# Kernel tuning notes

Hardware: AMD Instinct MI355X
Metric: run time of the kernel (lower is better)

## Reference

```python
import jax, jax.numpy as jnp
import numpy as np

N = 100000      # nodes
E = 1600000     # edges
F_IN = 256      # num_features
H = 128         # hidden_dim
C = 16          # num_classes
LOG_SIGMA0 = float(np.log(0.1))  # prior_sigma = 0.1


def setup_inputs() -> dict:
    key = jax.random.key(0)
    ks = jax.random.split(key, 8)
    x = jax.random.normal(ks[0], (N, F_IN), jnp.float32)
    edge_index = jax.random.randint(ks[1], (2, E), 0, N, dtype=jnp.int64)
    # GCNConv linear weight + bias
    W = jax.random.normal(ks[2], (F_IN, H), jnp.float32) / np.float32(np.sqrt(F_IN))
    gcn_b = jnp.zeros((H,), jnp.float32)
    # BayesLinear params (mu + log_sigma) and fixed sampled noise eps
    w_mu = jax.random.normal(ks[3], (C, H), jnp.float32) / np.float32(np.sqrt(H))
    w_log_sigma = jnp.full((C, H), LOG_SIGMA0, jnp.float32)
    b_mu = jnp.zeros((C,), jnp.float32)
    b_log_sigma = jnp.full((C,), LOG_SIGMA0, jnp.float32)
    eps_w = jax.random.normal(ks[4], (C, H), jnp.float32)
    eps_b = jax.random.normal(ks[5], (C,), jnp.float32)
    return {"x": x, "edge_index": edge_index, "W": W, "gcn_b": gcn_b,
            "w_mu": w_mu, "w_log_sigma": w_log_sigma,
            "b_mu": b_mu, "b_log_sigma": b_log_sigma,
            "eps_w": eps_w, "eps_b": eps_b}


def reference(x, edge_index, W, gcn_b, w_mu, w_log_sigma, b_mu, b_log_sigma, eps_w, eps_b):
    n = x.shape[0]
    # --- GCNConv: add self-loops, symmetric deg^{-1/2} normalization ---
    loop = jnp.arange(n, dtype=edge_index.dtype)
    src = jnp.concatenate([edge_index[0], loop])  # message source j
    dst = jnp.concatenate([edge_index[1], loop])  # aggregation target i
    deg = jax.ops.segment_sum(jnp.ones_like(dst, dtype=x.dtype), dst, num_segments=n)
    deg_inv_sqrt = jnp.where(deg > 0, jax.lax.rsqrt(deg), 0.0)
    norm = deg_inv_sqrt[src] * deg_inv_sqrt[dst]            # [E+N]
    h = x @ W                                               # [N,H] transform first
    msg = h[src] * norm[:, None]                            # [E+N,H] gather
    agg = jax.ops.segment_sum(msg, dst, num_segments=n)     # [N,H] scatter-add
    agg = agg + gcn_b
    # --- ReLU; dropout is identity in eval mode ---
    a = jax.nn.relu(agg)
    # --- BayesLinear: w = mu + exp(log_sigma) * eps ---
    w = w_mu + jnp.exp(w_log_sigma) * eps_w                 # [C,H]
    b = b_mu + jnp.exp(b_log_sigma) * eps_b                 # [C]
    logits = a @ w.T + b                                    # [N,C]
    return jax.nn.log_softmax(logits, axis=1)
```

## Files before the change

### kernel.cpp

```cpp
#include <hip/hip_runtime.h>
#include <hip/hip_bf16.h>

#define N_NODES 100000
#define F_IN    256
#define H_DIM   128
#define C_CLS   16
#define NB_SCAN ((N_NODES + 255) / 256)
#define NSHARD  8
#define SHARD_W ((N_NODES + NSHARD - 1) / NSHARD)

typedef __attribute__((ext_vector_type(8))) short  short8;
typedef __attribute__((ext_vector_type(4))) float  float4v;
typedef __attribute__((ext_vector_type(4))) unsigned short ushort4v;

__device__ __forceinline__ float b2f(ushort u) {
    union { unsigned int i; float f; } v;
    v.i = ((unsigned int)u) << 16;
    return v.f;
}

__device__ __forceinline__ ushort f2b(float f) {
    unsigned int x = __float_as_uint(f);
    unsigned int r = (x + 0x7FFFu + ((x >> 16) & 1u)) >> 16;
    return (ushort)r;
}

__device__ __forceinline__ float ldsel(const void* p, int i, int f32f) {
    return f32f ? ((const float*)p)[i] : b2f(((const ushort*)p)[i]);
}

__global__ __launch_bounds__(64) void sniff(const ushort* __restrict__ x,
                                            const int* __restrict__ ei,
                                            int* __restrict__ flags) {
    int lane = threadIdx.x;
    int cnt_bf = 0;
#pragma unroll
    for (int j = 0; j < 4; ++j) {
        ushort u = x[lane * 4 + j];
        int e = (u >> 7) & 0xFF;
        if ((e >= 100 && e <= 140) || (u & 0x7FFF) == 0) cnt_bf++;
    }
    int zodd = (ei[2 * lane + 1] == 0) ? 1 : 0;
#pragma unroll
    for (int off = 32; off >= 1; off >>= 1) {
        cnt_bf += __shfl_xor(cnt_bf, off, 64);
        zodd   += __shfl_xor(zodd,   off, 64);
    }
    if (lane == 0) {
        flags[0] = (cnt_bf < 230) ? 1 : 0;
        flags[1] = (zodd  >= 32) ? 1 : 0;
    }
}

__global__ __launch_bounds__(256) void prep_w(const int* __restrict__ flags,
                                              const void* __restrict__ W_any,
                                              ushort* __restrict__ wtg) {
    const int f32f = flags[0];
    const int n = blockIdx.x;
    const int k = threadIdx.x;
    float v = f32f ? ((const float*)W_any)[k * H_DIM + n]
                   : b2f(((const ushort*)W_any)[k * H_DIM + n]);
    wtg[n * F_IN + k] = f2b(v);
}

__global__ __launch_bounds__(512) void make_w(const int* __restrict__ flags,
                                              const void* __restrict__ w_mu,
                                              const void* __restrict__ w_ls,
                                              const void* __restrict__ eps_w,
                                              const void* __restrict__ b_mu,
                                              const void* __restrict__ b_ls,
                                              const void* __restrict__ eps_b,
                                              const void* __restrict__ gcn_b,
                                              ushort* __restrict__ whi,
                                              ushort* __restrict__ wlo,
                                              float* __restrict__ bias16,
                                              float* __restrict__ gcnb_f) {
    const int f32f = flags[0];
    const int t = threadIdx.x;
#pragma unroll
    for (int i = t; i < C_CLS * H_DIM; i += 512) {
        float v = ldsel(w_mu, i, f32f) + __expf(ldsel(w_ls, i, f32f)) * ldsel(eps_w, i, f32f);
        ushort h = f2b(v);
        whi[i] = h;
        wlo[i] = f2b(v - b2f(h));
    }
    if (t < C_CLS)
        bias16[t] = ldsel(b_mu, t, f32f) + __expf(ldsel(b_ls, t, f32f)) * ldsel(eps_b, t, f32f);
    if (t < H_DIM)
        gcnb_f[t] = ldsel(gcn_b, t, f32f);
}

__global__ __launch_bounds__(256) void prep(const int* __restrict__ flags,
                                            const int* __restrict__ ei,
                                            int* __restrict__ cnt, int E) {
    int e = blockIdx.x * 256 + threadIdx.x;
    if (e >= E) return;
    int d = flags[1] ? ei[2L * E + 2L * e] : ei[(long)E + e];
    atomicAdd(&cnt[d], 1);
}

__global__ __launch_bounds__(256) void scan1(const int* __restrict__ cnt,
                                             int* __restrict__ offs,
                                             int* __restrict__ bsum) {
    __shared__ int sd[256];
    int t = threadIdx.x;
    int i = blockIdx.x * 256 + t;
    int v = (i < N_NODES) ? cnt[i] : 0;
    sd[t] = v;
    __syncthreads();
#pragma unroll
    for (int d = 1; d < 256; d <<= 1) {
        int add = (t >= d) ? sd[t - d] : 0;
        __syncthreads();
        sd[t] += add;
        __syncthreads();
    }
    if (i < N_NODES) offs[i] = sd[t] - v;
    if (t == 255) bsum[blockIdx.x] = sd[255];
}

__global__ __launch_bounds__(512) void scan2(const int* __restrict__ bsum,
                                             int* __restrict__ boff) {
    __shared__ int sd[512];
    int t = threadIdx.x;
    int v = (t < NB_SCAN) ? bsum[t] : 0;
    sd[t] = v;
    __syncthreads();
#pragma unroll
    for (int d = 1; d < 512; d <<= 1) {
        int add = (t >= d) ? sd[t - d] : 0;
        __syncthreads();
        sd[t] += add;
        __syncthreads();
    }
    if (t < NB_SCAN) boff[t] = sd[t] - v;
}

__global__ __launch_bounds__(256) void scan3(int* __restrict__ offs,
                                             const int* __restrict__ boff,
                                             const int* __restrict__ cnt,
                                             int* __restrict__ cursor,
                                             float* __restrict__ dis, int E) {
    int i = blockIdx.x * 256 + threadIdx.x;
    if (i == 0) offs[N_NODES] = E;
    if (i >= N_NODES) return;
    int off = offs[i] + boff[i >> 8];
    offs[i] = off;
    cursor[i] = off;
    dis[i] = rsqrtf((float)(cnt[i] + 1));
}

__global__ __launch_bounds__(256) void build_perm(const int* __restrict__ flags,
                                                  const int* __restrict__ ei,
                                                  int* __restrict__ cursor,
                                                  int* __restrict__ perm, int E) {
    const int shard = blockIdx.x & (NSHARD - 1);
    const int jb    = blockIdx.x >> 3;
    const int nb    = gridDim.x >> 3;
    const int lo = shard * SHARD_W;
    const int hi = lo + SHARD_W;
    const int i64 = flags[1];
    for (long e = (long)jb * 256 + threadIdx.x; e < E; e += (long)nb * 256) {
        int d = i64 ? ei[2L * E + 2L * e] : ei[(long)E + e];
        if (d >= lo && d < hi) {
            int s = i64 ? ei[2L * e] : ei[e];
            int slot = atomicAdd(&cursor[d], 1);
            perm[slot] = s;
        }
    }
}

__global__ __launch_bounds__(256) void gemm_xw(const int* __restrict__ flags,
                                               const void* __restrict__ x_any,
                                               const ushort* __restrict__ wtg,
                                               const float* __restrict__ dis,
                                               ushort* __restrict__ hout) {
    __shared__ __align__(16) ushort wt[128 * 128];
    const int f32f = flags[0];

    const int tid  = threadIdx.x;
    const int lane = tid & 63;
    const int quad = lane >> 4;
    const int lm   = lane & 15;
    const int wave = tid >> 6;

    const int rbase = blockIdx.x * 64 + wave * 16;
    int arow = rbase + lm;
    if (arow >= N_NODES) arow = N_NODES - 1;
    const float*  xrf = (const float*) x_any + (size_t)arow * F_IN;
    const ushort* xrb = (const ushort*)x_any + (size_t)arow * F_IN;

    float4v acc[8];
#pragma unroll
    for (int c = 0; c < 8; ++c) acc[c] = (float4v){0.f, 0.f, 0.f, 0.f};

    for (int hh = 0; hh < 2; ++hh) {
        if (hh) __syncthreads();
#pragma unroll
        for (int it = 0; it < 8; ++it) {
            int flat = (it * 256 + tid) * 8;
            int col  = flat >> 7;
            int kloc = flat & 127;
            short8 v = *(const short8*)(wtg + col * F_IN + hh * 128 + kloc);
            int dst = ((col << 7) | kloc) ^ ((col & 7) << 3);
            *(short8*)(wt + dst) = v;
        }
        __syncthreads();
#pragma unroll
        for (int s = 0; s < 4; ++s) {
            int klocal = s * 32 + quad * 8;
            short8 afrag;
            if (f32f) {
                const float* p = xrf + hh * 128 + klocal;
                float4 u0 = *(const float4*)p;
                float4 u1 = *(const float4*)(p + 4);
                afrag[0] = (short)f2b(u0.x); afrag[1] = (short)f2b(u0.y);
                afrag[2] = (short)f2b(u0.z); afrag[3] = (short)f2b(u0.w);
                afrag[4] = (short)f2b(u1.x); afrag[5] = (short)f2b(u1.y);
                afrag[6] = (short)f2b(u1.z); afrag[7] = (short)f2b(u1.w);
            } else {
                afrag = *(const short8*)(xrb + hh * 128 + klocal);
            }
#pragma unroll
            for (int c = 0; c < 8; ++c) {
                int colr = c * 16 + lm;
                int src = ((colr << 7) | klocal) ^ ((lm & 7) << 3);
                short8 bfrag = *(const short8*)(wt + src);
                acc[c] = __builtin_amdgcn_mfma_f32_16x16x32_bf16(afrag, bfrag, acc[c], 0, 0, 0);
            }
        }
    }
    float dv[4];
#pragma unroll
    for (int r = 0; r < 4; ++r) {
        int node = rbase + quad * 4 + r;
        dv[r] = (node < N_NODES) ? dis[node] : 0.f;
    }
#pragma unroll
    for (int c = 0; c < 8; ++c) {
        int col = c * 16 + lm;
#pragma unroll
        for (int r = 0; r < 4; ++r) {
            int node = rbase + quad * 4 + r;
            if (node < N_NODES) hout[(size_t)node * H_DIM + col] = f2b(acc[c][r] * dv[r]);
        }
    }
}

__global__ __launch_bounds__(256) void gather_relu(const int* __restrict__ offs,
                                                   const int* __restrict__ perm,
                                                   const float* __restrict__ dis,
                                                   const ushort* __restrict__ hb,
                                                   const float* __restrict__ gcnb_f,
                                                   ushort* __restrict__ aout) {
    const int lane = threadIdx.x & 63;
    const int node = blockIdx.x * 4 + (threadIdx.x >> 6);
    if (node >= N_NODES) return;

    const int off0 = __builtin_amdgcn_readfirstlane(offs[node]);
    const int deg  = __builtin_amdgcn_readfirstlane(offs[node + 1]) - off0;
    const int* pp = perm + off0;

    float ax = 0.f, ay = 0.f;
    const int full = deg & ~15;
    for (int base = 0; base < full; base += 16) {
#pragma unroll
        for (int k = 0; k < 16; ++k) {
            int sk = pp[base + k];
            uint u = *((const uint*)(hb + (size_t)sk * H_DIM) + lane);
            ax += __uint_as_float(u << 16);
            ay += __uint_as_float(u & 0xFFFF0000u);
        }
    }
    {
        const int nb = deg - full;
#pragma unroll
        for (int k = 0; k < 16; ++k) {
            int   sk = 0;
            float wk = 0.f;
            if (k < nb) { sk = pp[full + k]; wk = 1.f; }
            uint u = *((const uint*)(hb + (size_t)sk * H_DIM) + lane);
            ax = fmaf(wk, __uint_as_float(u << 16),         ax);
            ay = fmaf(wk, __uint_as_float(u & 0xFFFF0000u), ay);
        }
    }

    const float dd = dis[node];
    uint us = *((const uint*)(hb + (size_t)node * H_DIM) + lane);
    float2 gb = *(const float2*)(gcnb_f + 2 * lane);
    ax = (ax + __uint_as_float(us << 16))         * dd + gb.x;
    ay = (ay + __uint_as_float(us & 0xFFFF0000u)) * dd + gb.y;
    ax = fmaxf(ax, 0.f);
    ay = fmaxf(ay, 0.f);
    uint pack = (uint)f2b(ax) | ((uint)f2b(ay) << 16);
    *((uint*)(aout + (size_t)node * H_DIM) + lane) = pack;
}

__global__ __launch_bounds__(256) void final_linear(const int* __restrict__ flags,
                                                    const ushort* __restrict__ a,
                                                    const ushort* __restrict__ whi,
                                                    const ushort* __restrict__ wlo,
                                                    const float* __restrict__ bias16,
                                                    void* __restrict__ out) {
    const int f32f = flags[0];
    const int lane = threadIdx.x & 63;
    const int wave = threadIdx.x >> 6;
    const int n0 = (blockIdx.x * 4 + wave) * 16;
    if (n0 >= N_NODES) return;
    const int lm = lane & 15, quad = lane >> 4;

    const ushort* arow = a   + (size_t)(n0 + lm) * H_DIM + quad * 8;
    const ushort* bh   = whi + lm * H_DIM + quad * 8;
    const ushort* bl   = wlo + lm * H_DIM + quad * 8;

    float4v acc = (float4v){0.f, 0.f, 0.f, 0.f};
#pragma unroll
    for (int s = 0; s < 4; ++s) {
        short8 af = *(const short8*)(arow + s * 32);
        short8 b0 = *(const short8*)(bh   + s * 32);
        short8 b1 = *(const short8*)(bl   + s * 32);
        acc = __builtin_amdgcn_mfma_f32_16x16x32_bf16(af, b0, acc, 0, 0, 0);
        acc = __builtin_amdgcn_mfma_f32_16x16x32_bf16(af, b1, acc, 0, 0, 0);
    }

    const float bias = bias16[lm];
    float p[4], m[4], ss[4];
#pragma unroll
    for (int r = 0; r < 4; ++r) { p[r] = acc[r] + bias; m[r] = p[r]; }
#pragma unroll
    for (int off = 1; off < 16; off <<= 1)
#pragma unroll
        for (int r = 0; r < 4; ++r) m[r] = fmaxf(m[r], __shfl_xor(m[r], off, 64));
#pragma unroll
    for (int r = 0; r < 4; ++r) ss[r] = __expf(p[r] - m[r]);
#pragma unroll
    for (int off = 1; off < 16; off <<= 1)
#pragma unroll
        for (int r = 0; r < 4; ++r) ss[r] += __shfl_xor(ss[r], off, 64);

    if (f32f) {
        float* op = (float*)out;
#pragma unroll
        for (int r = 0; r < 4; ++r)
            op[(size_t)(n0 + quad * 4 + r) * C_CLS + lm] = p[r] - m[r] - __logf(ss[r]);
    } else {
        ushort* op = (ushort*)out;
#pragma unroll
        for (int r = 0; r < 4; ++r)
            op[(size_t)(n0 + quad * 4 + r) * C_CLS + lm] = f2b(p[r] - m[r] - __logf(ss[r]));
    }
}

extern "C" void kernel_launch(void* const* d_in, const int* in_sizes, int n_in,
                              void* d_out, int out_size, void* d_ws, size_t ws_size,
                              hipStream_t stream) {
    const int E = in_sizes[1] / 2;

    char* wp = (char*)d_ws;
    auto alloc = [&](size_t bytes) -> char* {
        char* p = wp; wp += (bytes + 511) & ~(size_t)511; return p;
    };
    int*    flags  = (int*)   alloc(64);
    ushort* hb     = (ushort*)alloc((size_t)N_NODES * H_DIM * 2);
    ushort* aout   = (ushort*)alloc((size_t)N_NODES * H_DIM * 2);
    int*    cnt    = (int*)   alloc((size_t)N_NODES * 4);
    int*    offs   = (int*)   alloc((size_t)(N_NODES + 1) * 4);
    int*    cursor = (int*)   alloc((size_t)N_NODES * 4);
    int*    bsum   = (int*)   alloc((size_t)NB_SCAN * 4);
    int*    boff   = (int*)   alloc((size_t)NB_SCAN * 4);
    float*  dis    = (float*) alloc((size_t)N_NODES * 4);
    int*    perm   = (int*)   alloc((size_t)E * 4);
    ushort* wtg    = (ushort*)alloc((size_t)H_DIM * F_IN * 2);
    ushort* whi    = (ushort*)alloc((size_t)C_CLS * H_DIM * 2);
    ushort* wlo    = (ushort*)alloc((size_t)C_CLS * H_DIM * 2);
    float*  bias16 = (float*) alloc((size_t)C_CLS * 4);
    float*  gcnb_f = (float*) alloc((size_t)H_DIM * 4);

    sniff<<<1, 64, 0, stream>>>((const ushort*)d_in[0], (const int*)d_in[1], flags);
    prep_w<<<H_DIM, 256, 0, stream>>>(flags, d_in[2], wtg);
    make_w<<<1, 512, 0, stream>>>(flags, d_in[4], d_in[5], d_in[8],
                                  d_in[6], d_in[7], d_in[9], d_in[3],
                                  whi, wlo, bias16, gcnb_f);
    (void)hipMemsetAsync(cnt, 0, (size_t)N_NODES * 4, stream);
    prep<<<(E + 255) / 256, 256, 0, stream>>>(flags, (const int*)d_in[1], cnt, E);
    scan1<<<NB_SCAN, 256, 0, stream>>>(cnt, offs, bsum);
    scan2<<<1, 512, 0, stream>>>(bsum, boff);
    scan3<<<NB_SCAN, 256, 0, stream>>>(offs, boff, cnt, cursor, dis, E);
    build_perm<<<2048, 256, 0, stream>>>(flags, (const int*)d_in[1], cursor, perm, E);
    gemm_xw<<<(N_NODES + 63) / 64, 256, 0, stream>>>(flags, d_in[0], wtg, dis, hb);
    gather_relu<<<(N_NODES + 3) / 4, 256, 0, stream>>>(offs, perm, dis, hb, gcnb_f, aout);
    final_linear<<<(N_NODES / C_CLS + 3) / 4, 256, 0, stream>>>(flags, aout, whi, wlo, bias16, (void*)d_out);
}
```

Before: 413.8 us.

## Merge weight-prep kernels and double rows per wave in XW GEMM

Combines the two small parameter-prep kernels into one launch, with an extra block handling the Bayesian weight sampling and biases. The XW GEMM now has each wave compute 32 rows using two accumulator sets, so every B fragment read from LDS is reused twice and the W tile load into shared memory is amortised over 128 rows per block. This halves the GEMM grid but raises register pressure (16 accumulators) and may reduce occupancy.

```diff
diff --git a/kernel.cpp b/kernel.cpp
--- a/kernel.cpp
+++ b/kernel.cpp
@@ -52,33 +52,31 @@
     }
 }
 
-__global__ __launch_bounds__(256) void prep_w(const int* __restrict__ flags,
-                                              const void* __restrict__ W_any,
-                                              ushort* __restrict__ wtg) {
-    const int f32f = flags[0];
-    const int n = blockIdx.x;
-    const int k = threadIdx.x;
-    float v = f32f ? ((const float*)W_any)[k * H_DIM + n]
-                   : b2f(((const ushort*)W_any)[k * H_DIM + n]);
-    wtg[n * F_IN + k] = f2b(v);
-}
-
-__global__ __launch_bounds__(512) void make_w(const int* __restrict__ flags,
-                                              const void* __restrict__ w_mu,
-                                              const void* __restrict__ w_ls,
-                                              const void* __restrict__ eps_w,
-                                              const void* __restrict__ b_mu,
-                                              const void* __restrict__ b_ls,
-                                              const void* __restrict__ eps_b,
-                                              const void* __restrict__ gcn_b,
-                                              ushort* __restrict__ whi,
-                                              ushort* __restrict__ wlo,
-                                              float* __restrict__ bias16,
-                                              float* __restrict__ gcnb_f) {
+__global__ __launch_bounds__(256) void prep_params(const int* __restrict__ flags,
+                                                   const void* __restrict__ W_any,
+                                                   ushort* __restrict__ wtg,
+                                                   const void* __restrict__ w_mu,
+                                                   const void* __restrict__ w_ls,
+                                                   const void* __restrict__ eps_w,
+                                                   const void* __restrict__ b_mu,
+                                                   const void* __restrict__ b_ls,
+                                                   const void* __restrict__ eps_b,
+                                                   const void* __restrict__ gcn_b,
+                                                   ushort* __restrict__ whi,
+                                                   ushort* __restrict__ wlo,
+                                                   float* __restrict__ bias16,
+                                                   float* __restrict__ gcnb_f) {
     const int f32f = flags[0];
     const int t = threadIdx.x;
-#pragma unroll
-    for (int i = t; i < C_CLS * H_DIM; i += 512) {
+    if (blockIdx.x < H_DIM) {
+        const int n = blockIdx.x;
+        float v = f32f ? ((const float*)W_any)[t * H_DIM + n]
+                       : b2f(((const ushort*)W_any)[t * H_DIM + n]);
+        wtg[n * F_IN + t] = f2b(v);
+        return;
+    }
+#pragma unroll
+    for (int i = t; i < C_CLS * H_DIM; i += 256) {
         float v = ldsel(w_mu, i, f32f) + __expf(ldsel(w_ls, i, f32f)) * ldsel(eps_w, i, f32f);
         ushort h = f2b(v);
         whi[i] = h;
@@ -184,15 +182,22 @@
     const int lm   = lane & 15;
     const int wave = tid >> 6;
 
-    const int rbase = blockIdx.x * 64 + wave * 16;
-    int arow = rbase + lm;
-    if (arow >= N_NODES) arow = N_NODES - 1;
-    const float*  xrf = (const float*) x_any + (size_t)arow * F_IN;
-    const ushort* xrb = (const ushort*)x_any + (size_t)arow * F_IN;
-
-    float4v acc[8];
-#pragma unroll
-    for (int c = 0; c < 8; ++c) acc[c] = (float4v){0.f, 0.f, 0.f, 0.f};
+    const int rbase = blockIdx.x * 128 + wave * 32;
+    int arow0 = rbase + lm;
+    int arow1 = rbase + 16 + lm;
+    if (arow0 >= N_NODES) arow0 = N_NODES - 1;
+    if (arow1 >= N_NODES) arow1 = N_NODES - 1;
+    const float*  xrf0 = (const float*) x_any + (size_t)arow0 * F_IN;
+    const float*  xrf1 = (const float*) x_any + (size_t)arow1 * F_IN;
+    const ushort* xrb0 = (const ushort*)x_any + (size_t)arow0 * F_IN;
+    const ushort* xrb1 = (const ushort*)x_any + (size_t)arow1 * F_IN;
+
+    float4v acc0[8], acc1[8];
+#pragma unroll
+    for (int c = 0; c < 8; ++c) {
+        acc0[c] = (float4v){0.f, 0.f, 0.f, 0.f};
+        acc1[c] = (float4v){0.f, 0.f, 0.f, 0.f};
+    }
 
     for (int hh = 0; hh < 2; ++hh) {
         if (hh) __syncthreads();
@@ -209,40 +214,53 @@
 #pragma unroll
         for (int s = 0; s < 4; ++s) {
             int klocal = s * 32 + quad * 8;
-            short8 afrag;
+            short8 afrag0, afrag1;
             if (f32f) {
-                const float* p = xrf + hh * 128 + klocal;
-                float4 u0 = *(const float4*)p;
-                float4 u1 = *(const float4*)(p + 4);
-                afrag[0] = (short)f2b(u0.x); afrag[1] = (short)f2b(u0.y);
-                afrag[2] = (short)f2b(u0.z); afrag[3] = (short)f2b(u0.w);
-                afrag[4] = (short)f2b(u1.x); afrag[5] = (short)f2b(u1.y);
-                afrag[6] = (short)f2b(u1.z); afrag[7] = (short)f2b(u1.w);
+                const float* p0 = xrf0 + hh * 128 + klocal;
+                const float* p1 = xrf1 + hh * 128 + klocal;
+                float4 u0 = *(const float4*)p0;
+                float4 u1 = *(const float4*)(p0 + 4);
+                float4 u2 = *(const float4*)p1;
+                float4 u3 = *(const float4*)(p1 + 4);
+                afrag0[0] = (short)f2b(u0.x); afrag0[1] = (short)f2b(u0.y);
+                afrag0[2] = (short)f2b(u0.z); afrag0[3] = (short)f2b(u0.w);
+                afrag0[4] = (short)f2b(u1.x); afrag0[5] = (short)f2b(u1.y);
+                afrag0[6] = (short)f2b(u1.z); afrag0[7] = (short)f2b(u1.w);
+                afrag1[0] = (short)f2b(u2.x); afrag1[1] = (short)f2b(u2.y);
+                afrag1[2] = (short)f2b(u2.z); afrag1[3] = (short)f2b(u2.w);
+                afrag1[4] = (short)f2b(u3.x); afrag1[5] = (short)f2b(u3.y);
+                afrag1[6] = (short)f2b(u3.z); afrag1[7] = (short)f2b(u3.w);
             } else {
-                afrag = *(const short8*)(xrb + hh * 128 + klocal);
+                afrag0 = *(const short8*)(xrb0 + hh * 128 + klocal);
+                afrag1 = *(const short8*)(xrb1 + hh * 128 + klocal);
             }
 #pragma unroll
             for (int c = 0; c < 8; ++c) {
                 int colr = c * 16 + lm;
                 int src = ((colr << 7) | klocal) ^ ((lm & 7) << 3);
                 short8 bfrag = *(const short8*)(wt + src);
-                acc[c] = __builtin_amdgcn_mfma_f32_16x16x32_bf16(afrag, bfrag, acc[c], 0, 0, 0);
+                acc0[c] = __builtin_amdgcn_mfma_f32_16x16x32_bf16(afrag0, bfrag, acc0[c], 0, 0, 0);
+                acc1[c] = __builtin_amdgcn_mfma_f32_16x16x32_bf16(afrag1, bfrag, acc1[c], 0, 0, 0);
             }
         }
     }
-    float dv[4];
+    float dv0[4], dv1[4];
 #pragma unroll
     for (int r = 0; r < 4; ++r) {
-        int node = rbase + quad * 4 + r;
-        dv[r] = (node < N_NODES) ? dis[node] : 0.f;
+        int n0 = rbase + quad * 4 + r;
+        int n1 = rbase + 16 + quad * 4 + r;
+        dv0[r] = (n0 < N_NODES) ? dis[n0] : 0.f;
+        dv1[r] = (n1 < N_NODES) ? dis[n1] : 0.f;
     }
 #pragma unroll
     for (int c = 0; c < 8; ++c) {
         int col = c * 16 + lm;
 #pragma unroll
         for (int r = 0; r < 4; ++r) {
-            int node = rbase + quad * 4 + r;
-            if (node < N_NODES) hout[(size_t)node * H_DIM + col] = f2b(acc[c][r] * dv[r]);
+            int n0 = rbase + quad * 4 + r;
+            int n1 = rbase + 16 + quad * 4 + r;
+            if (n0 < N_NODES) hout[(size_t)n0 * H_DIM + col] = f2b(acc0[c][r] * dv0[r]);
+            if (n1 < N_NODES) hout[(size_t)n1 * H_DIM + col] = f2b(acc1[c][r] * dv1[r]);
         }
     }
 }
@@ -377,8 +395,8 @@
     float*  gcnb_f = (float*) alloc((size_t)H_DIM * 4);
 
     sniff<<<1, 64, 0, stream>>>((const ushort*)d_in[0], (const int*)d_in[1], flags);
-    prep_w<<<H_DIM, 256, 0, stream>>>(flags, d_in[2], wtg);
-    make_w<<<1, 512, 0, stream>>>(flags, d_in[4], d_in[5], d_in[8],
+    prep_params<<<H_DIM + 1, 256, 0, stream>>>(flags, d_in[2], wtg,
+                                  d_in[4], d_in[5], d_in[8],
                                   d_in[6], d_in[7], d_in[9], d_in[3],
                                   whi, wlo, bias16, gcnb_f);
     (void)hipMemsetAsync(cnt, 0, (size_t)N_NODES * 4, stream);
@@ -387,7 +405,7 @@
     scan2<<<1, 512, 0, stream>>>(bsum, boff);
     scan3<<<NB_SCAN, 256, 0, stream>>>(offs, boff, cnt, cursor, dis, E);
     build_perm<<<2048, 256, 0, stream>>>(flags, (const int*)d_in[1], cursor, perm, E);
-    gemm_xw<<<(N_NODES + 63) / 64, 256, 0, stream>>>(flags, d_in[0], wtg, dis, hb);
+    gemm_xw<<<(N_NODES + 127) / 128, 256, 0, stream>>>(flags, d_in[0], wtg, dis, hb);
     gather_relu<<<(N_NODES + 3) / 4, 256, 0, stream>>>(offs, perm, dis, hb, gcnb_f, aout);
     final_linear<<<(N_NODES / C_CLS + 3) / 4, 256, 0, stream>>>(flags, aout, whi, wlo, bias16, (void*)d_out);
 }
```

New measurement: 414.5 us. Within noise of the previous version (+0.2%).
